# Performance work log

Hardware: AMD Instinct MI355X
Metric: run time of the kernel (lower is better)

## Reference

```python
import jax, jax.numpy as jnp
import numpy as np

N_NODES = 50000


def gin_conv(x, src, dst, W, b, eps=0.0):
    # GINConv: nn((1+eps)*x_i + sum_{j in N(i)} x_j)
    agg = jax.ops.segment_sum(x[src], dst, num_segments=N_NODES)  # [N, D]
    h = (1.0 + eps) * x + agg
    return h @ W + b


def setup_inputs() -> dict:
    key = jax.random.key(0)
    ks = jax.random.split(key, 8)
    n, e = N_NODES, 800000
    d_in, d_h, d_out = 128, 128, 64
    feature = jax.random.normal(ks[0], (n, d_in), dtype=jnp.float32)
    edge_index = jax.random.randint(ks[1], (2, e), 0, n, dtype=jnp.int64)
    s1 = 1.0 / np.sqrt(d_in)
    sh = 1.0 / np.sqrt(d_h)
    W1 = jax.random.normal(ks[2], (d_in, d_h), dtype=jnp.float32) * s1
    b1 = jnp.zeros((d_h,), dtype=jnp.float32)
    Wh = jax.random.normal(ks[3], (d_h, d_h), dtype=jnp.float32) * sh
    bh = jnp.zeros((d_h,), dtype=jnp.float32)
    Wo = jax.random.normal(ks[4], (d_h, d_out), dtype=jnp.float32) * sh
    bo = jnp.zeros((d_out,), dtype=jnp.float32)
    return {"feature": feature, "edge_index": edge_index, "W1": W1, "b1": b1,
            "Wh": Wh, "bh": bh, "Wo": Wo, "bo": bo}


def reference(feature, edge_index, W1, b1, Wh, bh, Wo, bo):
    src, dst = edge_index[0], edge_index[1]
    x = gin_conv(feature, src, dst, W1, b1)
    x = jax.nn.relu(x)
    # one hidden layer (layer_num=3); dropout disabled (eval)
    x = gin_conv(x, src, dst, Wh, bh)
    x = jax.nn.relu(x)
    x = gin_conv(x, src, dst, Wo, bo)
    return jax.nn.log_softmax(x, axis=1)
```

## Files before the change

### kernel.cpp

```cpp
#include <hip/hip_runtime.h>

typedef short short8 __attribute__((ext_vector_type(8)));
typedef float f32x4 __attribute__((ext_vector_type(4)));


__device__ inline unsigned short f2bf(float f) {
    union { float f; unsigned u; } v; v.f = f;
    unsigned r = v.u + 0x7fffu + ((v.u >> 16) & 1u);
    return (unsigned short)(r >> 16);
}
__device__ inline unsigned pack2(float a, float b) {
    return (unsigned)f2bf(a) | ((unsigned)f2bf(b) << 16);
}
__device__ inline float bflo(unsigned u) { union { unsigned q; float f; } c; c.q = u << 16; return c.f; }
__device__ inline float bfhi(unsigned u) { union { unsigned q; float f; } c; c.q = u & 0xffff0000u; return c.f; }


#define EPB 2048
#define NE 8
#define BSH 9
#define MAXBKT 128
#define DCAP 10240

__global__ __launch_bounds__(256) void binA(const int* __restrict__ src, const int* __restrict__ dst,
                                            int* __restrict__ cnt2d, int e, int nbkt, int nblk) {
    __shared__ int hist[MAXBKT];
    int t = threadIdx.x, blk = blockIdx.x;
    for (int b = t; b < nbkt; b += 256) hist[b] = 0;
    __syncthreads();
    int base = blk * EPB;
#pragma unroll
    for (int j = 0; j < NE; j++) {
        int idx = base + t + 256 * j;
        if (idx < e) atomicAdd(&hist[dst[idx] >> BSH], 1);
    }
    __syncthreads();
    for (int b = t; b < nbkt; b += 256) cnt2d[b * nblk + blk] = hist[b];
}

__global__ __launch_bounds__(512) void scanB1(int* __restrict__ cnt2d, int* __restrict__ totals, int nblk) {
    __shared__ int s[512];
    int t = threadIdx.x, b = blockIdx.x;
    int v = (t < nblk) ? cnt2d[b * nblk + t] : 0;
    s[t] = v;
    __syncthreads();
    for (int off = 1; off < 512; off <<= 1) {
        int u = (t >= off) ? s[t - off] : 0;
        __syncthreads();
        s[t] += u;
        __syncthreads();
    }
    if (t < nblk) cnt2d[b * nblk + t] = s[t] - v;
    if (t == nblk - 1) totals[b] = s[t];
}

__global__ __launch_bounds__(128) void scanB2(const int* __restrict__ totals, int* __restrict__ bbase,
                                              int* __restrict__ row_ptr, int nbkt, int n, int e) {
    __shared__ int s[128];
    int t = threadIdx.x;
    int v = (t < nbkt) ? totals[t] : 0;
    s[t] = v;
    __syncthreads();
    for (int off = 1; off < 128; off <<= 1) {
        int u = (t >= off) ? s[t - off] : 0;
        __syncthreads();
        s[t] += u;
        __syncthreads();
    }
    if (t < nbkt) bbase[t] = s[t] - v;
    if (t == 0) row_ptr[n] = e;
}

__global__ __launch_bounds__(256) void binC(const int* __restrict__ src, const int* __restrict__ dst,
                                            const int* __restrict__ cnt2d, const int* __restrict__ bbase,
                                            unsigned* __restrict__ pairs, int e, int nbkt, int nblk) {
    __shared__ int hist[MAXBKT], loff[MAXBKT], cur[MAXBKT], gb[MAXBKT];
    __shared__ int sc[256];
    __shared__ unsigned sorted[EPB];
    int t = threadIdx.x, blk = blockIdx.x;
    for (int b = t; b < nbkt; b += 256) hist[b] = 0;
    __syncthreads();
    int base = blk * EPB;
    int cnt = min(EPB, e - base);
    unsigned packed[NE];
    int bb[NE];
#pragma unroll
    for (int j = 0; j < NE; j++) {
        int idx = base + t + 256 * j;
        bb[j] = -1;
        if (idx < e) {
            unsigned s0 = (unsigned)src[idx], d = (unsigned)dst[idx];
            int b = (int)(d >> BSH);
            bb[j] = b;
            packed[j] = s0 | ((d & ((1u << BSH) - 1)) << 16) | ((unsigned)b << 25);
            atomicAdd(&hist[b], 1);
        }
    }
    __syncthreads();
    int v = (t < nbkt) ? hist[t] : 0;
    sc[t] = v;
    __syncthreads();
    for (int off = 1; off < 256; off <<= 1) {
        int u = (t >= off) ? sc[t - off] : 0;
        __syncthreads();
        sc[t] += u;
        __syncthreads();
    }
    if (t < nbkt) {
        int ex = sc[t] - v;
        loff[t] = ex;
        cur[t] = ex;
        gb[t] = bbase[t] + cnt2d[t * nblk + blk];
    }
    __syncthreads();
#pragma unroll
    for (int j = 0; j < NE; j++) {
        if (bb[j] >= 0) {
            int r = atomicAdd(&cur[bb[j]], 1);
            sorted[r] = packed[j];
        }
    }
    __syncthreads();
    for (int i = t; i < cnt; i += 256) {
        unsigned w = sorted[i];
        int b = (int)(w >> 25);
        pairs[gb[b] + (i - loff[b])] = w;
    }
}

__global__ __launch_bounds__(512) void buildD(const unsigned* __restrict__ pairs,
                                              const int* __restrict__ totals, const int* __restrict__ bbase,
                                              int* __restrict__ row_ptr, unsigned short* __restrict__ csr, int n) {
    __shared__ int hist[512], off[512];
    __shared__ unsigned short lcsr[DCAP];
    int t = threadIdx.x, b = blockIdx.x;
    int cnt = totals[b], base = bbase[b];
    hist[t] = 0;
    __syncthreads();
    for (int i = t; i < cnt; i += 512)
        atomicAdd(&hist[(pairs[base + i] >> 16) & 511], 1);
    __syncthreads();
    int v = hist[t];
    off[t] = v;
    __syncthreads();
    for (int o = 1; o < 512; o <<= 1) {
        int u = (t >= o) ? off[t - o] : 0;
        __syncthreads();
        off[t] += u;
        __syncthreads();
    }
    int excl = off[t] - v;
    int node = (b << BSH) + t;
    if (node < n) row_ptr[node] = base + excl;
    __syncthreads();
    hist[t] = excl;
    __syncthreads();
    for (int i = t; i < cnt; i += 512) {
        unsigned w = pairs[base + i];
        int r = atomicAdd(&hist[(w >> 16) & 511], 1);
        if (r < DCAP) lcsr[r] = (unsigned short)(w & 0xFFFFu);
    }
    __syncthreads();
    int lim = min(cnt, DCAP);
    for (int i = t; i < lim; i += 512) csr[base + i] = lcsr[i];
}


__global__ void cvt_bf16_kernel(const float4* __restrict__ in, uint2* __restrict__ out, int nf4) {
    int i = blockIdx.x * 256 + threadIdx.x;
    if (i < nf4) {
        float4 v = in[i];
        out[i] = make_uint2(pack2(v.x, v.y), pack2(v.z, v.w));
    }
}

__global__ void wt_all(const float* __restrict__ W1, const float* __restrict__ Wh, const float* __restrict__ Wo,
                       unsigned short* __restrict__ W1t, unsigned short* __restrict__ Wht,
                       unsigned short* __restrict__ Wot) {
    int i = blockIdx.x * 256 + threadIdx.x;
    if (i < 16384) {
        int k = i >> 7, nn = i & 127;
        W1t[nn * 128 + k] = f2bf(W1[i]);
    } else if (i < 32768) {
        int j = i - 16384, k = j >> 7, nn = j & 127;
        Wht[nn * 128 + k] = f2bf(Wh[j]);
    } else if (i < 40960) {
        int j = i - 32768, k = j >> 6, nn = j & 63;
        Wot[nn * 128 + k] = f2bf(Wo[j]);
    }
}


#define ACC8(vv)                                     \
    acc[0] += bflo(vv.x); acc[1] += bfhi(vv.x);      \
    acc[2] += bflo(vv.y); acc[3] += bfhi(vv.y);      \
    acc[4] += bflo(vv.z); acc[5] += bfhi(vv.z);      \
    acc[6] += bflo(vv.w); acc[7] += bfhi(vv.w);

template <int TPN>
__global__ __launch_bounds__(256) void agg_kernel(
    const uint4* __restrict__ x, uint4* __restrict__ outp,
    const int* __restrict__ row_ptr, const unsigned short* __restrict__ csr, int n) {
    int gt = blockIdx.x * 256 + threadIdx.x;
    int node = gt / TPN, lane = gt % TPN;
    if (node >= n) return;
    size_t base = (size_t)node * TPN + lane;
    uint4 s0 = x[base];
    float acc[8] = { bflo(s0.x), bfhi(s0.x), bflo(s0.y), bfhi(s0.y),
                     bflo(s0.z), bfhi(s0.z), bflo(s0.w), bfhi(s0.w) };
    int beg = row_ptr[node], end = row_ptr[node + 1];
    int ed = beg;
    for (; ed + 4 <= end; ed += 4) {
        int i0 = csr[ed], i1 = csr[ed + 1], i2 = csr[ed + 2], i3 = csr[ed + 3];
        uint4 v0 = x[(size_t)i0 * TPN + lane];
        uint4 v1 = x[(size_t)i1 * TPN + lane];
        uint4 v2 = x[(size_t)i2 * TPN + lane];
        uint4 v3 = x[(size_t)i3 * TPN + lane];
        ACC8(v0) ACC8(v1) ACC8(v2) ACC8(v3)
    }
    for (; ed < end; ++ed) {
        uint4 v0 = x[(size_t)csr[ed] * TPN + lane];
        ACC8(v0)
    }
    uint4 o;
    o.x = pack2(acc[0], acc[1]); o.y = pack2(acc[2], acc[3]);
    o.z = pack2(acc[4], acc[5]); o.w = pack2(acc[6], acc[7]);
    outp[base] = o;
}

__global__ __launch_bounds__(256) void agg_lsm(
    const uint4* __restrict__ x, float* __restrict__ out,
    const int* __restrict__ row_ptr, const unsigned short* __restrict__ csr,
    const float* __restrict__ bo, int n) {
    int gt = blockIdx.x * 256 + threadIdx.x;
    int node = gt >> 3, lane = gt & 7;
    if (node >= n) return;
    size_t base = (size_t)node * 8 + lane;
    uint4 s0 = x[base];
    float acc[8] = { bflo(s0.x), bfhi(s0.x), bflo(s0.y), bfhi(s0.y),
                     bflo(s0.z), bfhi(s0.z), bflo(s0.w), bfhi(s0.w) };
    int beg = row_ptr[node], end = row_ptr[node + 1];
    int ed = beg;
    for (; ed + 4 <= end; ed += 4) {
        int i0 = csr[ed], i1 = csr[ed + 1], i2 = csr[ed + 2], i3 = csr[ed + 3];
        uint4 v0 = x[(size_t)i0 * 8 + lane];
        uint4 v1 = x[(size_t)i1 * 8 + lane];
        uint4 v2 = x[(size_t)i2 * 8 + lane];
        uint4 v3 = x[(size_t)i3 * 8 + lane];
        ACC8(v0) ACC8(v1) ACC8(v2) ACC8(v3)
    }
    for (; ed < end; ++ed) {
        uint4 v0 = x[(size_t)csr[ed] * 8 + lane];
        ACC8(v0)
    }
    const float4* bo4 = (const float4*)bo;
    float4 bA = bo4[lane * 2], bB = bo4[lane * 2 + 1];
    acc[0] += bA.x; acc[1] += bA.y; acc[2] += bA.z; acc[3] += bA.w;
    acc[4] += bB.x; acc[5] += bB.y; acc[6] += bB.z; acc[7] += bB.w;
    float m = acc[0];
#pragma unroll
    for (int j = 1; j < 8; j++) m = fmaxf(m, acc[j]);
#pragma unroll
    for (int off = 1; off < 8; off <<= 1) m = fmaxf(m, __shfl_xor(m, off, 64));
    float s = 0.f;
#pragma unroll
    for (int j = 0; j < 8; j++) s += __expf(acc[j] - m);
#pragma unroll
    for (int off = 1; off < 8; off <<= 1) s += __shfl_xor(s, off, 64);
    float ls = m + __logf(s);
    float4 o0 = make_float4(acc[0] - ls, acc[1] - ls, acc[2] - ls, acc[3] - ls);
    float4 o1 = make_float4(acc[4] - ls, acc[5] - ls, acc[6] - ls, acc[7] - ls);
    float4* op = (float4*)(out + (size_t)node * 64 + lane * 8);
    op[0] = o0;
    op[1] = o1;
}


template <int OUT, bool RELU, bool BIAS>
__global__ __launch_bounds__(256) void gemm_mfma(
    const short8* __restrict__ A, const short8* __restrict__ Bt,
    const float* __restrict__ bias, unsigned short* __restrict__ outp, int n) {
    constexpr int NT = OUT / 16;
    int wid = threadIdx.x >> 6, lane = threadIdx.x & 63;
    int lm = lane & 15, lq = lane >> 4;
    int r0 = blockIdx.x * 64 + wid * 16;

    int arow = r0 + lm;
    if (arow >= n) arow = n - 1;
    const short8* Ar = A + (size_t)arow * 16;
    short8 a[4];
#pragma unroll
    for (int kc = 0; kc < 4; kc++) a[kc] = Ar[kc * 4 + lq];

    f32x4 acc[NT];
#pragma unroll
    for (int nt = 0; nt < NT; nt++) acc[nt] = (f32x4){0.f, 0.f, 0.f, 0.f};

#pragma unroll
    for (int nt = 0; nt < NT; nt++) {
        const short8* Br = Bt + (size_t)(nt * 16 + lm) * 16;
#pragma unroll
        for (int kc = 0; kc < 4; kc++)
            acc[nt] = __builtin_amdgcn_mfma_f32_16x16x32_bf16(a[kc], Br[kc * 4 + lq], acc[nt], 0, 0, 0);
    }

#pragma unroll
    for (int nt = 0; nt < NT; nt++) {
        int col = nt * 16 + lm;
        float bv = BIAS ? bias[col] : 0.f;
#pragma unroll
        for (int i = 0; i < 4; i++) {
            int row = r0 + lq * 4 + i;
            if (row < n) {
                float v = acc[nt][i] + bv;
                if (RELU) v = fmaxf(v, 0.f);
                outp[(size_t)row * OUT + col] = f2bf(v);
            }
        }
    }
}


extern "C" void kernel_launch(void* const* d_in, const int* in_sizes, int n_in,
                              void* d_out, int out_size, void* d_ws, size_t ws_size,
                              hipStream_t stream) {
    const float* feature = (const float*)d_in[0];
    const int*   edges   = (const int*)d_in[1];
    const float* W1 = (const float*)d_in[2];
    const float* b1 = (const float*)d_in[3];
    const float* Wh = (const float*)d_in[4];
    const float* bh = (const float*)d_in[5];
    const float* Wo = (const float*)d_in[6];
    const float* bo = (const float*)d_in[7];

    int n = in_sizes[0] / 128;
    int e = in_sizes[1] / 2;
    const int* src = edges;
    const int* dst = edges + e;

    int nbkt = (n + 511) >> BSH;
    int nblk = (e + EPB - 1) / EPB;

    char* ws = (char*)d_ws;
    auto take = [&](size_t bytes) {
        char* p = ws;
        ws += (bytes + 255) & ~(size_t)255;
        return p;
    };
    int* cnt2d   = (int*)take((size_t)nbkt * nblk * 4);
    int* totals  = (int*)take((size_t)nbkt * 4);
    int* bbase   = (int*)take((size_t)(nbkt + 1) * 4);
    int* row_ptr = (int*)take((size_t)(n + 1) * 4);
    unsigned* pairs = (unsigned*)take((size_t)e * 4);
    unsigned short* csr = (unsigned short*)take((size_t)e * 2);
    unsigned short* featb = (unsigned short*)take((size_t)n * 128 * 2);
    unsigned short* aggb  = (unsigned short*)take((size_t)n * 128 * 2);
    unsigned short* hb    = (unsigned short*)take((size_t)n * 128 * 2);
    unsigned short* yb    = (unsigned short*)take((size_t)n * 64 * 2);
    unsigned short* W1t = (unsigned short*)take(128 * 128 * 2);
    unsigned short* Wht = (unsigned short*)take(128 * 128 * 2);
    unsigned short* Wot = (unsigned short*)take(64 * 128 * 2);

    binA<<<nblk, 256, 0, stream>>>(src, dst, cnt2d, e, nbkt, nblk);
    scanB1<<<nbkt, 512, 0, stream>>>(cnt2d, totals, nblk);
    scanB2<<<1, 128, 0, stream>>>(totals, bbase, row_ptr, nbkt, n, e);
    binC<<<nblk, 256, 0, stream>>>(src, dst, cnt2d, bbase, pairs, e, nbkt, nblk);
    buildD<<<nbkt, 512, 0, stream>>>(pairs, totals, bbase, row_ptr, csr, n);

    cvt_bf16_kernel<<<(n * 32 + 255) / 256, 256, 0, stream>>>(
        (const float4*)feature, (uint2*)featb, n * 32);
    wt_all<<<160, 256, 0, stream>>>(W1, Wh, Wo, W1t, Wht, Wot);

    int gemm_blocks = (n + 63) / 64;

    agg_kernel<16><<<(n * 16 + 255) / 256, 256, 0, stream>>>(
        (const uint4*)featb, (uint4*)aggb, row_ptr, csr, n);
    gemm_mfma<128, true, true><<<gemm_blocks, 256, 0, stream>>>(
        (const short8*)aggb, (const short8*)W1t, b1, hb, n);

    agg_kernel<16><<<(n * 16 + 255) / 256, 256, 0, stream>>>(
        (const uint4*)hb, (uint4*)aggb, row_ptr, csr, n);
    gemm_mfma<128, true, true><<<gemm_blocks, 256, 0, stream>>>(
        (const short8*)aggb, (const short8*)Wht, bh, hb, n);

    gemm_mfma<64, false, false><<<gemm_blocks, 256, 0, stream>>>(
        (const short8*)hb, (const short8*)Wot, nullptr, yb, n);
    agg_lsm<<<(n * 8 + 255) / 256, 256, 0, stream>>>(
        (const uint4*)yb, (float*)d_out, row_ptr, csr, bo, n);
}
```

Measured before the change: 249.3 us.

## Fuse neighbor aggregation with MFMA GEMM per layer and chain output GEMM

Replaces separate aggregation and GEMM kernels with a fused kernel that gathers 16 nodes' neighbor sums into shared memory and immediately multiplies by the weight matrix with MFMA. The second layer also applies the output projection in the same kernel, avoiding writing and re-reading intermediate activations. Gather loops are unrolled to 8 edges for more outstanding loads. The tradeoff is smaller GEMM tiles with weight reloads per 16-row block and a barrier between gather and compute.

New measurement: 221.1 us. 1.13x faster.

```diff
diff --git a/kernel.cpp b/kernel.cpp
--- a/kernel.cpp
+++ b/kernel.cpp
@@ -197,36 +197,116 @@
     acc[4] += bflo(vv.z); acc[5] += bfhi(vv.z);      \
     acc[6] += bflo(vv.w); acc[7] += bfhi(vv.w);
 
-template <int TPN>
-__global__ __launch_bounds__(256) void agg_kernel(
-    const uint4* __restrict__ x, uint4* __restrict__ outp,
-    const int* __restrict__ row_ptr, const unsigned short* __restrict__ csr, int n) {
-    int gt = blockIdx.x * 256 + threadIdx.x;
-    int node = gt / TPN, lane = gt % TPN;
-    if (node >= n) return;
-    size_t base = (size_t)node * TPN + lane;
-    uint4 s0 = x[base];
-    float acc[8] = { bflo(s0.x), bfhi(s0.x), bflo(s0.y), bfhi(s0.y),
-                     bflo(s0.z), bfhi(s0.z), bflo(s0.w), bfhi(s0.w) };
-    int beg = row_ptr[node], end = row_ptr[node + 1];
-    int ed = beg;
-    for (; ed + 4 <= end; ed += 4) {
-        int i0 = csr[ed], i1 = csr[ed + 1], i2 = csr[ed + 2], i3 = csr[ed + 3];
-        uint4 v0 = x[(size_t)i0 * TPN + lane];
-        uint4 v1 = x[(size_t)i1 * TPN + lane];
-        uint4 v2 = x[(size_t)i2 * TPN + lane];
-        uint4 v3 = x[(size_t)i3 * TPN + lane];
-        ACC8(v0) ACC8(v1) ACC8(v2) ACC8(v3)
-    }
-    for (; ed < end; ++ed) {
-        uint4 v0 = x[(size_t)csr[ed] * TPN + lane];
-        ACC8(v0)
-    }
-    uint4 o;
-    o.x = pack2(acc[0], acc[1]); o.y = pack2(acc[2], acc[3]);
-    o.z = pack2(acc[4], acc[5]); o.w = pack2(acc[6], acc[7]);
-    outp[base] = o;
-}
+
+template <bool SECOND>
+__global__ __launch_bounds__(256) void fused_layer(
+    const uint4* __restrict__ x, const int* __restrict__ row_ptr,
+    const unsigned short* __restrict__ csr,
+    const short8* __restrict__ Bt, const float* __restrict__ bias,
+    unsigned short* __restrict__ out_h,
+    const short8* __restrict__ Bt2,
+    unsigned short* __restrict__ out_y,
+    int n) {
+    __shared__ unsigned short As[16][136];
+    __shared__ unsigned short Hs[SECOND ? 16 : 1][SECOND ? 136 : 1];
+
+    int t = threadIdx.x;
+    int nl = t >> 4, chunk = t & 15;
+    int r0 = blockIdx.x * 16;
+    int node = r0 + nl;
+
+    float acc[8] = {0.f, 0.f, 0.f, 0.f, 0.f, 0.f, 0.f, 0.f};
+    if (node < n) {
+        size_t base = (size_t)node * 16 + chunk;
+        uint4 s0 = x[base];
+        ACC8(s0)
+        int beg = row_ptr[node], end = row_ptr[node + 1];
+        int ed = beg;
+        for (; ed + 8 <= end; ed += 8) {
+            int idx[8];
+#pragma unroll
+            for (int j = 0; j < 8; j++) idx[j] = csr[ed + j];
+            uint4 v[8];
+#pragma unroll
+            for (int j = 0; j < 8; j++) v[j] = x[(size_t)idx[j] * 16 + chunk];
+#pragma unroll
+            for (int j = 0; j < 8; j++) { ACC8(v[j]) }
+        }
+        for (; ed + 4 <= end; ed += 4) {
+            int i0 = csr[ed], i1 = csr[ed + 1], i2 = csr[ed + 2], i3 = csr[ed + 3];
+            uint4 v0 = x[(size_t)i0 * 16 + chunk];
+            uint4 v1 = x[(size_t)i1 * 16 + chunk];
+            uint4 v2 = x[(size_t)i2 * 16 + chunk];
+            uint4 v3 = x[(size_t)i3 * 16 + chunk];
+            ACC8(v0) ACC8(v1) ACC8(v2) ACC8(v3)
+        }
+        for (; ed < end; ++ed) {
+            uint4 v0 = x[(size_t)csr[ed] * 16 + chunk];
+            ACC8(v0)
+        }
+    }
+    uint4 packed;
+    packed.x = pack2(acc[0], acc[1]); packed.y = pack2(acc[2], acc[3]);
+    packed.z = pack2(acc[4], acc[5]); packed.w = pack2(acc[6], acc[7]);
+    ((uint4*)&As[nl][0])[chunk] = packed;
+    __syncthreads();
+
+    int wid = t >> 6, lane = t & 63;
+    int lm = lane & 15, lq = lane >> 4;
+
+    short8 a[4];
+#pragma unroll
+    for (int kc = 0; kc < 4; kc++)
+        a[kc] = *(const short8*)&As[lm][kc * 32 + lq * 8];
+
+    f32x4 hacc[2];
+#pragma unroll
+    for (int nt = 0; nt < 2; nt++) hacc[nt] = (f32x4){0.f, 0.f, 0.f, 0.f};
+#pragma unroll
+    for (int nt = 0; nt < 2; nt++) {
+        int ct = wid * 2 + nt;
+        const short8* Br = Bt + (size_t)(ct * 16 + lm) * 16;
+#pragma unroll
+        for (int kc = 0; kc < 4; kc++)
+            hacc[nt] = __builtin_amdgcn_mfma_f32_16x16x32_bf16(a[kc], Br[kc * 4 + lq], hacc[nt], 0, 0, 0);
+    }
+
+#pragma unroll
+    for (int nt = 0; nt < 2; nt++) {
+        int col = (wid * 2 + nt) * 16 + lm;
+        float bv = bias[col];
+#pragma unroll
+        for (int i = 0; i < 4; i++) {
+            int row = r0 + lq * 4 + i;
+            float v = fmaxf(hacc[nt][i] + bv, 0.f);
+            if (SECOND) {
+                Hs[lq * 4 + i][col] = f2bf(v);
+            } else if (row < n) {
+                out_h[(size_t)row * 128 + col] = f2bf(v);
+            }
+        }
+    }
+
+    if (SECOND) {
+        __syncthreads();
+        short8 a2[4];
+#pragma unroll
+        for (int kc = 0; kc < 4; kc++)
+            a2[kc] = *(const short8*)&Hs[lm][kc * 32 + lq * 8];
+        f32x4 yacc = (f32x4){0.f, 0.f, 0.f, 0.f};
+        const short8* Br2 = Bt2 + (size_t)(wid * 16 + lm) * 16;
+#pragma unroll
+        for (int kc = 0; kc < 4; kc++)
+            yacc = __builtin_amdgcn_mfma_f32_16x16x32_bf16(a2[kc], Br2[kc * 4 + lq], yacc, 0, 0, 0);
+        int col = wid * 16 + lm;
+#pragma unroll
+        for (int i = 0; i < 4; i++) {
+            int row = r0 + lq * 4 + i;
+            if (row < n) out_y[(size_t)row * 64 + col] = f2bf(yacc[i]);
+        }
+    }
+}
+
 
 __global__ __launch_bounds__(256) void agg_lsm(
     const uint4* __restrict__ x, float* __restrict__ out,
@@ -241,6 +321,16 @@
                      bflo(s0.z), bfhi(s0.z), bflo(s0.w), bfhi(s0.w) };
     int beg = row_ptr[node], end = row_ptr[node + 1];
     int ed = beg;
+    for (; ed + 8 <= end; ed += 8) {
+        int idx[8];
+#pragma unroll
+        for (int j = 0; j < 8; j++) idx[j] = csr[ed + j];
+        uint4 v[8];
+#pragma unroll
+        for (int j = 0; j < 8; j++) v[j] = x[(size_t)idx[j] * 8 + lane];
+#pragma unroll
+        for (int j = 0; j < 8; j++) { ACC8(v[j]) }
+    }
     for (; ed + 4 <= end; ed += 4) {
         int i0 = csr[ed], i1 = csr[ed + 1], i2 = csr[ed + 2], i3 = csr[ed + 3];
         uint4 v0 = x[(size_t)i0 * 8 + lane];
@@ -273,51 +363,6 @@
     float4* op = (float4*)(out + (size_t)node * 64 + lane * 8);
     op[0] = o0;
     op[1] = o1;
-}
-
-
-template <int OUT, bool RELU, bool BIAS>
-__global__ __launch_bounds__(256) void gemm_mfma(
-    const short8* __restrict__ A, const short8* __restrict__ Bt,
-    const float* __restrict__ bias, unsigned short* __restrict__ outp, int n) {
-    constexpr int NT = OUT / 16;
-    int wid = threadIdx.x >> 6, lane = threadIdx.x & 63;
-    int lm = lane & 15, lq = lane >> 4;
-    int r0 = blockIdx.x * 64 + wid * 16;
-
-    int arow = r0 + lm;
-    if (arow >= n) arow = n - 1;
-    const short8* Ar = A + (size_t)arow * 16;
-    short8 a[4];
-#pragma unroll
-    for (int kc = 0; kc < 4; kc++) a[kc] = Ar[kc * 4 + lq];
-
-    f32x4 acc[NT];
-#pragma unroll
-    for (int nt = 0; nt < NT; nt++) acc[nt] = (f32x4){0.f, 0.f, 0.f, 0.f};
-
-#pragma unroll
-    for (int nt = 0; nt < NT; nt++) {
-        const short8* Br = Bt + (size_t)(nt * 16 + lm) * 16;
-#pragma unroll
-        for (int kc = 0; kc < 4; kc++)
-            acc[nt] = __builtin_amdgcn_mfma_f32_16x16x32_bf16(a[kc], Br[kc * 4 + lq], acc[nt], 0, 0, 0);
-    }
-
-#pragma unroll
-    for (int nt = 0; nt < NT; nt++) {
-        int col = nt * 16 + lm;
-        float bv = BIAS ? bias[col] : 0.f;
-#pragma unroll
-        for (int i = 0; i < 4; i++) {
-            int row = r0 + lq * 4 + i;
-            if (row < n) {
-                float v = acc[nt][i] + bv;
-                if (RELU) v = fmaxf(v, 0.f);
-                outp[(size_t)row * OUT + col] = f2bf(v);
-            }
-        }
-    }
 }
 
 
@@ -354,7 +399,6 @@
     unsigned* pairs = (unsigned*)take((size_t)e * 4);
     unsigned short* csr = (unsigned short*)take((size_t)e * 2);
     unsigned short* featb = (unsigned short*)take((size_t)n * 128 * 2);
-    unsigned short* aggb  = (unsigned short*)take((size_t)n * 128 * 2);
     unsigned short* hb    = (unsigned short*)take((size_t)n * 128 * 2);
     unsigned short* yb    = (unsigned short*)take((size_t)n * 64 * 2);
     unsigned short* W1t = (unsigned short*)take(128 * 128 * 2);
@@ -371,20 +415,16 @@
         (const float4*)feature, (uint2*)featb, n * 32);
     wt_all<<<160, 256, 0, stream>>>(W1, Wh, Wo, W1t, Wht, Wot);
 
-    int gemm_blocks = (n + 63) / 64;
-
-    agg_kernel<16><<<(n * 16 + 255) / 256, 256, 0, stream>>>(
-        (const uint4*)featb, (uint4*)aggb, row_ptr, csr, n);
-    gemm_mfma<128, true, true><<<gemm_blocks, 256, 0, stream>>>(
-        (const short8*)aggb, (const short8*)W1t, b1, hb, n);
-
-    agg_kernel<16><<<(n * 16 + 255) / 256, 256, 0, stream>>>(
-        (const uint4*)hb, (uint4*)aggb, row_ptr, csr, n);
-    gemm_mfma<128, true, true><<<gemm_blocks, 256, 0, stream>>>(
-        (const short8*)aggb, (const short8*)Wht, bh, hb, n);
-
-    gemm_mfma<64, false, false><<<gemm_blocks, 256, 0, stream>>>(
-        (const short8*)hb, (const short8*)Wot, nullptr, yb, n);
+    int fblocks = (n + 15) / 16;
+
+    fused_layer<false><<<fblocks, 256, 0, stream>>>(
+        (const uint4*)featb, row_ptr, csr, (const short8*)W1t, b1,
+        hb, nullptr, nullptr, n);
+
+    fused_layer<true><<<fblocks, 256, 0, stream>>>(
+        (const uint4*)hb, row_ptr, csr, (const short8*)Wht, bh,
+        nullptr, (const short8*)Wot, yb, n);
+
     agg_lsm<<<(n * 8 + 255) / 256, 256, 0, stream>>>(
         (const uint4*)yb, (float*)d_out, row_ptr, csr, bo, n);
 }
```
